# Kernel optimization log

Hardware: AMD Instinct MI355X
Metric: run time of the kernel (lower is better)

The kernel has to match this reference:

```python
import jax, jax.numpy as jnp
import numpy as np

ITER_STEPS = 2


def setup_inputs() -> dict:
    key = jax.random.key(0)
    ks = jax.random.split(key, 9)
    B, N, D, E = 64, 256, 512, 10  # batch, nodes, node_dim, edge types
    node = jax.random.normal(ks[0], (B, N, D), dtype=jnp.float32)
    node_mask = jax.random.randint(ks[1], (B, N), 0, 2).astype(jnp.int32)
    adj = jax.random.randint(ks[2], (E, B, N, N), 0, 2).astype(jnp.int32)
    s = 0.02
    W_nw = jax.random.normal(ks[3], (1, D), dtype=jnp.float32) * s   # node weight fc [out=1, in=D]
    b_nw = jnp.zeros((1,), dtype=jnp.float32)
    W_self = jax.random.normal(ks[4], (D, D), dtype=jnp.float32) * s
    b_self = jnp.zeros((D,), dtype=jnp.float32)
    W_edge = jax.random.normal(ks[5], (E, D, D), dtype=jnp.float32) * s  # per-edge-type Linear (no bias)
    return {"node": node, "W_nw": W_nw, "b_nw": b_nw, "W_self": W_self,
            "b_self": b_self, "W_edge": W_edge, "node_mask": node_mask, "adj": adj}


def reference(node, W_nw, b_nw, W_self, b_self, W_edge, node_mask, adj):
    # node: [B,N,D]; node_mask: [B,N] int; adj: [E=10,B,N,N] int (binary)
    B, N, D = node.shape
    m = node_mask.astype(node.dtype)
    eye = jnp.eye(N, dtype=node.dtype)
    # dd_graph = mask outer-product with zeroed diagonal: [B,N,N]
    dd = m[:, None, :] * m[:, :, None] * (1.0 - eye)
    graphs = dd[None] * adj.astype(node.dtype)  # [E,B,N,N]
    # total neighbor count across all 10 edge types, clamped to >=1 (replace_masked_values)
    neigh = graphs.sum(axis=(0, 3))                       # [B,N]
    neigh = jnp.where(neigh >= 1.0, neigh, 1.0)
    all_weight = []
    for _ in range(ITER_STEPS):
        # (1) node relatedness gate
        w = jax.nn.sigmoid(node @ W_nw.T + b_nw)[..., 0]  # [B,N]
        all_weight.append(w)
        self_info = node @ W_self.T + b_self              # [B,N,D]
        # (2) per-edge-type projection + masked adjacency matmul, summed over edge types
        proj = jnp.einsum('bnk,edk->ebnd', node, W_edge)  # [E,B,N,D]
        masked_w = jnp.where(graphs != 0, w[None, :, None, :], 0.0)  # [E,B,N,N]
        agg = jnp.einsum('ebnm,ebmd->bnd', masked_w, proj)           # [B,N,D]
        # (3) update
        node = jax.nn.relu(self_info + agg / neigh[..., None])
    return node, jnp.stack(all_weight, axis=1)  # ([B,N,D], [B,ITER,N])
```

## Files before the change

### kernel.cpp

```cpp
#include <hip/hip_runtime.h>
#include <hip/hip_bf16.h>

#define BB 64
#define NN 256
#define DD 512
#define EE 10

typedef __bf16 bf16x8 __attribute__((ext_vector_type(8)));
typedef unsigned short ushort8v __attribute__((ext_vector_type(8)));
typedef unsigned int uint4v __attribute__((ext_vector_type(4)));
typedef float floatx4 __attribute__((ext_vector_type(4)));
typedef float floatx16 __attribute__((ext_vector_type(16)));

typedef __attribute__((address_space(3))) unsigned short lds_us;
typedef const __attribute__((address_space(1))) unsigned short glb_us;

__device__ __forceinline__ unsigned short f2b(float f) {
    union { float f; unsigned u; } x; x.f = f;
    unsigned r = x.u + 0x7FFFu + ((x.u >> 16) & 1u);
    return (unsigned short)(r >> 16);
}
__device__ __forceinline__ float b2f(unsigned short u) {
    union { unsigned u; float f; } x; x.u = ((unsigned)u) << 16;
    return x.f;
}

__global__ void k_wconv(const float* __restrict__ W_edge,
                        const float* __restrict__ W_self,
                        unsigned short* __restrict__ Wf) {
    int t = blockIdx.x * 256 + threadIdx.x;
    int lane  = t & 63;
    int kstep = (t >> 6) & 31;
    int cfg   = (t >> 11) & 15;
    int e     = t >> 15;
    int dout = cfg * 32 + (lane & 31);
    int k    = kstep * 16 + (lane >> 5) * 8;
    const float* src = (e < EE) ? (W_edge + ((size_t)e * DD + dout) * DD + k)
                                : (W_self + (size_t)dout * DD + k);
    ushort8v o;
    #pragma unroll
    for (int j = 0; j < 8; j++) o[j] = f2b(src[j]);
    *(ushort8v*)(Wf + (size_t)t * 8) = o;
}

__global__ void k_graph(const int* __restrict__ adj, const int* __restrict__ mask,
                        unsigned* __restrict__ packed, float* __restrict__ recip) {
    int b = blockIdx.x >> 8;
    int n = blockIdx.x & 255;
    int lane = threadIdx.x & 63;
    int wv   = threadIdx.x >> 6;
    int m = wv * 64 + lane;
    int ok = (mask[b * NN + n] != 0) & (mask[b * NN + m] != 0) & (m != n);
    __shared__ int cnt_s[4];
    int total = 0;
    #pragma unroll
    for (int e = 0; e < EE; e++) {
        int a = adj[(((size_t)e * BB + b) * NN + n) * NN + m];
        int bit = ok & (a != 0);
        unsigned long long bal = __ballot(bit);
        if (lane == 0) {
            unsigned* dst = packed + (((size_t)e * BB + b) * NN + n) * 8 + wv * 2;
            dst[0] = (unsigned)bal;
            dst[1] = (unsigned)(bal >> 32);
        }
        total += bit;
    }
    for (int off = 32; off; off >>= 1) total += __shfl_down(total, off);
    if (lane == 0) cnt_s[wv] = total;
    __syncthreads();
    if (threadIdx.x == 0) {
        int c = cnt_s[0] + cnt_s[1] + cnt_s[2] + cnt_s[3];
        recip[b * NN + n] = 1.0f / (float)(c < 1 ? 1 : c);
    }
}

template<int TI>
__global__ void k_gate(const float* __restrict__ xf, const unsigned short* __restrict__ xbin,
                       const float* __restrict__ W_nw, const float* __restrict__ b_nw,
                       float* __restrict__ w_buf, float* __restrict__ w_out) {
    int idx = blockIdx.x * 4 + (threadIdx.x >> 6);
    int lane = threadIdx.x & 63;
    size_t base = (size_t)idx * DD + lane * 8;
    const floatx4* wp = (const floatx4*)(W_nw + lane * 8);
    floatx4 w0 = wp[0], w1 = wp[1];
    float s = 0.f;
    if (TI == 0) {
        const floatx4* xp = (const floatx4*)(xf + base);
        floatx4 a0 = xp[0], a1 = xp[1];
        #pragma unroll
        for (int j = 0; j < 4; j++) s += a0[j] * w0[j] + a1[j] * w1[j];
    } else {
        ushort8v u = *(const ushort8v*)(xbin + base);
        #pragma unroll
        for (int j = 0; j < 8; j++) {
            float wj = (j < 4) ? w0[j] : w1[j - 4];
            s += b2f(u[j]) * wj;
        }
    }
    for (int off = 32; off; off >>= 1) s += __shfl_down(s, off);
    if (lane == 0) {
        float v = 1.f / (1.f + __expf(-(s + b_nw[0])));
        w_buf[idx] = v;
        int b = idx >> 8, n = idx & 255;
        w_out[(b * 2 + TI) * NN + n] = v;
    }
}

template<int TI>
__global__ void k_transf(const float* __restrict__ xf, const unsigned short* __restrict__ xbin,
                         const float* __restrict__ w_buf,
                         unsigned short* __restrict__ wTf, unsigned short* __restrict__ xb0) {
    int bid = blockIdx.x;
    int b  = bid >> 5;
    int nt = (bid >> 3) & 3;
    int dt = bid & 7;
    __shared__ float tile[64][65];
    __shared__ float ws[64];
    int j  = threadIdx.x & 63;
    int i0 = threadIdx.x >> 6;
    if (threadIdx.x < 64) ws[threadIdx.x] = w_buf[b * NN + nt * 64 + threadIdx.x];
    #pragma unroll
    for (int ii = 0; ii < 16; ii++) {
        int i = i0 * 16 + ii;
        size_t gi = ((size_t)b * NN + nt * 64 + i) * DD + dt * 64 + j;
        float v = (TI == 0) ? xf[gi] : b2f(xbin[gi]);
        tile[i][j] = v;
        if (TI == 0) xb0[gi] = f2b(v);
    }
    __syncthreads();
    int lane = threadIdx.x & 63;
    int l31 = lane & 31, hi = lane >> 5;
    #pragma unroll
    for (int cc = 0; cc < 2; cc++) {
        int c = cc * 4 + (threadIdx.x >> 6);
        int msl = c >> 1, dbl = c & 1;
        ushort8v o;
        #pragma unroll
        for (int jj = 0; jj < 8; jj++) {
            int m_loc = msl * 16 + hi * 8 + jj;
            int d_loc = dbl * 32 + l31;
            o[jj] = f2b(tile[m_loc][d_loc] * ws[m_loc]);
        }
        size_t idx = (((size_t)b * 16 + nt * 4 + msl) * 16 + dt * 2 + dbl) * 64 + lane;
        *(ushort8v*)(wTf + idx * 8) = o;
    }
}

template<int TI>
__global__ __launch_bounds__(512, 2)
void k2_heavy(const unsigned short* __restrict__ wTf,
              const unsigned short* __restrict__ xb,
              const unsigned short* __restrict__ Wf,
              const unsigned* __restrict__ packed,
              const float* __restrict__ recip,
              const float* __restrict__ b_self,
              unsigned short* __restrict__ out_bf16,
              float* __restrict__ out_f32) {
    __shared__ __attribute__((aligned(16))) unsigned short sWT[32 * 512];
    __shared__ __attribute__((aligned(16))) unsigned short sWf[2][32 * 512];
    __shared__ __attribute__((aligned(16))) unsigned short sT[128 * 76];

    int bid = blockIdx.x;
    int xcd = bid & 7;
    int ct  = xcd >> 2;
    int rtile = (bid >> 3) * 4 + (xcd & 3);
    int b = rtile >> 1, h = rtile & 1;
    int w = threadIdx.x >> 6, lane = threadIdx.x & 63;
    int rh = w >> 2;
    int cq = w & 3;
    int rbT = rh * 2 + (cq >> 1);
    int cbT = cq & 1;
    int l31 = lane & 31, hi = lane >> 5;

    float rn[16];
    #pragma unroll
    for (int rg = 0; rg < 16; rg++) {
        int rloc = (rg & 3) + 8 * (rg >> 2) + 4 * hi;
        rn[rg] = recip[b * NN + h * 128 + rbT * 32 + rloc];
    }

    floatx16 acc2[2][2];
    #pragma unroll
    for (int i = 0; i < 2; i++)
        #pragma unroll
        for (int jj = 0; jj < 2; jj++)
            #pragma unroll
            for (int q = 0; q < 16; q++) acc2[i][jj][q] = 0.f;

    auto stage_sWf = [&](int e, int dc, int buf) {
        #pragma unroll
        for (int it = 0; it < 4; it++) {
            int c = it * 8 + w;
            int cfl = c >> 2, kl = c & 3;
            const unsigned short* g = Wf +
                ((((size_t)e * 16 + ct * 8 + cfl) * 32 + dc * 4 + kl) * 64 + lane) * 8;
            __builtin_amdgcn_global_load_lds((glb_us*)g, (lds_us*)&sWf[buf][c * 512], 16, 0, 0);
        }
    };
    auto stage_sWT = [&](int dc) {
        #pragma unroll
        for (int it = 0; it < 4; it++) {
            int c = it * 8 + w;
            int msl = c >> 1, dbl = c & 1;
            const unsigned short* g = wTf +
                ((((size_t)b * 16 + msl) * 16 + dc * 2 + dbl) * 64 + lane) * 8;
            __builtin_amdgcn_global_load_lds((glb_us*)g, (lds_us*)&sWT[c * 512], 16, 0, 0);
        }
    };

    stage_sWT(0);
    stage_sWf(0, 0, 0);

    bf16x8 Bc[16];

    #pragma unroll 1
    for (int dc = 0; dc < 8; dc++) {
        #pragma unroll 1
        for (int e = 0; e <= EE; e++) {
            int s = dc * 11 + e;
            int cur = s & 1;
            asm volatile("s_waitcnt vmcnt(0)" ::: "memory");
            asm volatile("s_barrier" ::: "memory");

            unsigned pw[8];
            ushort8v xa[2][4];
            if (e < EE) {
                const uint4v* pp = (const uint4v*)(packed +
                    (((size_t)e * BB + b) * NN + h * 128 + rbT * 32 + l31) * 8);
                uint4v pa = pp[0], pb = pp[1];
                pw[0]=pa[0]; pw[1]=pa[1]; pw[2]=pa[2]; pw[3]=pa[3];
                pw[4]=pb[0]; pw[5]=pb[1]; pw[6]=pb[2]; pw[7]=pb[3];
            } else {
                #pragma unroll
                for (int ra = 0; ra < 2; ra++)
                    #pragma unroll
                    for (int ks = 0; ks < 4; ks++)
                        xa[ra][ks] = *(const ushort8v*)(xb +
                            ((size_t)(b * NN + h * 128 + rh * 64 + ra * 32 + l31)) * DD +
                            dc * 64 + ks * 16 + hi * 8);
            }
            if (s < 87) {
                int ne = e + 1, ndc = dc;
                if (ne == 11) { ne = 0; ndc = dc + 1; }
                stage_sWf(ne, ndc, cur ^ 1);
            }
            if (e == 1 && dc < 7) stage_sWT(dc + 1);

            if (e == 0) {
                #pragma unroll
                for (int ms = 0; ms < 16; ms++)
                    Bc[ms] = __builtin_bit_cast(bf16x8,
                        *(const ushort8v*)&sWT[((ms * 2 + cbT) * 64 + lane) * 8]);
            }

            if (e < EE) {
                floatx16 acc3;
                #pragma unroll
                for (int q = 0; q < 16; q++) acc3[q] = 0.f;
                #pragma unroll
                for (int ms = 0; ms < 16; ms++) {
                    unsigned byte = (pw[ms >> 1] >> ((((ms & 1) << 1) + hi) * 8)) & 0xFFu;
                    uint4v av;
                    #pragma unroll
                    for (int p = 0; p < 4; p++) {
                        unsigned b2 = (byte >> (2 * p)) & 3u;
                        av[p] = ((b2 & 1u) ? 0x3F80u : 0u) | ((b2 & 2u) ? 0x3F800000u : 0u);
                    }
                    acc3 = __builtin_amdgcn_mfma_f32_32x32x16_bf16(
                        __builtin_bit_cast(bf16x8, av), Bc[ms], acc3, 0, 0, 0);
                }
                #pragma unroll
                for (int rg = 0; rg < 16; rg++) {
                    int rloc = rbT * 32 + (rg & 3) + 8 * (rg >> 2) + 4 * hi;
                    sT[rloc * 76 + cbT * 32 + l31] = f2b(acc3[rg] * rn[rg]);
                }
                asm volatile("s_waitcnt lgkmcnt(0)" ::: "memory");
                asm volatile("s_barrier" ::: "memory");
            }
            #pragma unroll
            for (int ks = 0; ks < 4; ks++) {
                bf16x8 bfr[2];
                #pragma unroll
                for (int cb = 0; cb < 2; cb++)
                    bfr[cb] = __builtin_bit_cast(bf16x8,
                        *(const ushort8v*)&sWf[cur][(((cq * 2 + cb) * 4 + ks) * 64 + lane) * 8]);
                #pragma unroll
                for (int ra = 0; ra < 2; ra++) {
                    bf16x8 afr;
                    if (e < EE)
                        afr = __builtin_bit_cast(bf16x8, *(const ushort8v*)
                            &sT[(rh * 64 + ra * 32 + l31) * 76 + ks * 16 + hi * 8]);
                    else
                        afr = __builtin_bit_cast(bf16x8, xa[ra][ks]);
                    #pragma unroll
                    for (int cb = 0; cb < 2; cb++)
                        acc2[ra][cb] = __builtin_amdgcn_mfma_f32_32x32x16_bf16(
                            afr, bfr[cb], acc2[ra][cb], 0, 0, 0);
                }
            }
        }
    }
    #pragma unroll
    for (int cb = 0; cb < 2; cb++) {
        int col = ct * 256 + (cq * 2 + cb) * 32 + l31;
        float bs = b_self[col];
        #pragma unroll
        for (int ra = 0; ra < 2; ra++) {
            #pragma unroll
            for (int rg = 0; rg < 16; rg++) {
                int row = h * 128 + rh * 64 + ra * 32 + (rg & 3) + 8 * (rg >> 2) + 4 * hi;
                float v = acc2[ra][cb][rg] + bs;
                v = v > 0.f ? v : 0.f;
                size_t gi = ((size_t)b * NN + row) * DD + col;
                if (TI == 0) out_bf16[gi] = f2b(v);
                else         out_f32[gi] = v;
            }
        }
    }
}

extern "C" void kernel_launch(void* const* d_in, const int* in_sizes, int n_in,
                              void* d_out, int out_size, void* d_ws, size_t ws_size,
                              hipStream_t stream) {
    const float* node   = (const float*)d_in[0];
    const float* W_nw   = (const float*)d_in[1];
    const float* b_nw   = (const float*)d_in[2];
    const float* W_self = (const float*)d_in[3];
    const float* b_self = (const float*)d_in[4];
    const float* W_edge = (const float*)d_in[5];
    const int*   mask   = (const int*)d_in[6];
    const int*   adj    = (const int*)d_in[7];
    float* out = (float*)d_out;
    float* out_w = out + (size_t)BB * NN * DD;

    char* ws = (char*)d_ws;
    size_t off = 0;
    unsigned short* Wf    = (unsigned short*)(ws + off); off += (size_t)11 * DD * DD * 2;
    unsigned short* wTf   = (unsigned short*)(ws + off); off += (size_t)BB * DD * NN * 2;
    unsigned short* xb0   = (unsigned short*)(ws + off); off += (size_t)BB * NN * DD * 2;
    unsigned short* xb1   = (unsigned short*)(ws + off); off += (size_t)BB * NN * DD * 2;
    unsigned*       packed= (unsigned*)(ws + off);       off += (size_t)EE * BB * NN * 8 * 4;
    float*          recip = (float*)(ws + off);          off += (size_t)BB * NN * 4;
    float*          w_buf = (float*)(ws + off);          off += (size_t)BB * NN * 4;

    k_wconv<<<dim3(1408), dim3(256), 0, stream>>>(W_edge, W_self, Wf);
    k_graph<<<dim3(16384), dim3(256), 0, stream>>>(adj, mask, packed, recip);

    k_gate<0><<<dim3(4096), dim3(256), 0, stream>>>(node, nullptr, W_nw, b_nw, w_buf, out_w);
    k_transf<0><<<dim3(2048), dim3(256), 0, stream>>>(node, nullptr, w_buf, wTf, xb0);
    k2_heavy<0><<<dim3(256), dim3(512), 0, stream>>>(wTf, xb0, Wf, packed, recip, b_self, xb1, nullptr);

    k_gate<1><<<dim3(4096), dim3(256), 0, stream>>>(nullptr, xb1, W_nw, b_nw, w_buf, out_w);
    k_transf<1><<<dim3(2048), dim3(256), 0, stream>>>(nullptr, xb1, w_buf, wTf, xb0 );
    k2_heavy<1><<<dim3(256), dim3(512), 0, stream>>>(wTf, xb1, Wf, packed, recip, b_self, nullptr, out);
}
```

Measured before the change: 794.8 us.

## Reorder heavy kernel loop edge-major, double-buffer wT tiles and swizzle sT LDS

The fused aggregate-then-project kernel now loops edge type outermost and d-chunk innermost. The adjacency bit-pattern fragments are decoded into registers once per edge type, and the wT tile is double-buffered and reloaded every step instead of being held in registers across edges. The first MFMA now transposes operand roles so each wave writes packed bf16 pairs to an XOR-swizzled 64-wide sT buffer rather than a padded one, which cuts LDS bank conflicts and scalar stores. Block-to-batch mapping changes from the XCD-aware layout to a simple b-major one, which may affect L2 locality. The self path reads xb directly from global memory inside the MFMA loop.

```diff
diff --git a/kernel.cpp b/kernel.cpp
--- a/kernel.cpp
+++ b/kernel.cpp
@@ -9,6 +9,7 @@
 typedef __bf16 bf16x8 __attribute__((ext_vector_type(8)));
 typedef unsigned short ushort8v __attribute__((ext_vector_type(8)));
 typedef unsigned int uint4v __attribute__((ext_vector_type(4)));
+typedef unsigned int uint2v __attribute__((ext_vector_type(2)));
 typedef float floatx4 __attribute__((ext_vector_type(4)));
 typedef float floatx16 __attribute__((ext_vector_type(16)));
 
@@ -23,6 +24,10 @@
 __device__ __forceinline__ float b2f(unsigned short u) {
     union { unsigned u; float f; } x; x.u = ((unsigned)u) << 16;
     return x.f;
+}
+__device__ __forceinline__ unsigned pack_bf16(float a, float b) {
+    union { float f; unsigned u; } xa, xb2; xa.f = a; xb2.f = b;
+    return __builtin_amdgcn_perm(xa.u + 0x8000u, xb2.u + 0x8000u, 0x07060302u);
 }
 
 __global__ void k_wconv(const float* __restrict__ W_edge,
@@ -156,28 +161,23 @@
               const float* __restrict__ b_self,
               unsigned short* __restrict__ out_bf16,
               float* __restrict__ out_f32) {
-    __shared__ __attribute__((aligned(16))) unsigned short sWT[32 * 512];
+    __shared__ __attribute__((aligned(16))) unsigned short sWT[2][32 * 512];
     __shared__ __attribute__((aligned(16))) unsigned short sWf[2][32 * 512];
-    __shared__ __attribute__((aligned(16))) unsigned short sT[128 * 76];
+    __shared__ __attribute__((aligned(16))) unsigned short sT[128 * 64];
 
     int bid = blockIdx.x;
-    int xcd = bid & 7;
-    int ct  = xcd >> 2;
-    int rtile = (bid >> 3) * 4 + (xcd & 3);
-    int b = rtile >> 1, h = rtile & 1;
+    int b  = bid & 63;
+    int q  = bid >> 6;
+    int h  = q >> 1;
+    int ct = q & 1;
     int w = threadIdx.x >> 6, lane = threadIdx.x & 63;
-    int rh = w >> 2;
-    int cq = w & 3;
-    int rbT = rh * 2 + (cq >> 1);
-    int cbT = cq & 1;
     int l31 = lane & 31, hi = lane >> 5;
-
-    float rn[16];
-    #pragma unroll
-    for (int rg = 0; rg < 16; rg++) {
-        int rloc = (rg & 3) + 8 * (rg >> 2) + 4 * hi;
-        rn[rg] = recip[b * NN + h * 128 + rbT * 32 + rloc];
-    }
+    int s1_d  = w & 1;
+    int s1_nb = w >> 1;
+    int n1 = s1_nb * 32 + l31;
+    float rn = recip[b * NN + h * 128 + n1];
+    int nh2 = w & 1;
+    int dh4 = w >> 1;
 
     floatx16 acc2[2][2];
     #pragma unroll
@@ -185,131 +185,132 @@
         #pragma unroll
         for (int jj = 0; jj < 2; jj++)
             #pragma unroll
-            for (int q = 0; q < 16; q++) acc2[i][jj][q] = 0.f;
-
-    auto stage_sWf = [&](int e, int dc, int buf) {
+            for (int p = 0; p < 16; p++) acc2[i][jj][p] = 0.f;
+
+    auto stage_sWT = [&](int dc, int buf) {
         #pragma unroll
         for (int it = 0; it < 4; it++) {
             int c = it * 8 + w;
-            int cfl = c >> 2, kl = c & 3;
-            const unsigned short* g = Wf +
-                ((((size_t)e * 16 + ct * 8 + cfl) * 32 + dc * 4 + kl) * 64 + lane) * 8;
-            __builtin_amdgcn_global_load_lds((glb_us*)g, (lds_us*)&sWf[buf][c * 512], 16, 0, 0);
+            const unsigned short* g = wTf +
+                ((((size_t)b * 16 + (c >> 1)) * 16 + dc * 2 + (c & 1)) * 64 + lane) * 8;
+            __builtin_amdgcn_global_load_lds((glb_us*)g, (lds_us*)&sWT[buf][c * 512], 16, 0, 0);
         }
     };
-    auto stage_sWT = [&](int dc) {
+    auto stage_sWf = [&](int e, int dc, int buf) {
         #pragma unroll
         for (int it = 0; it < 4; it++) {
             int c = it * 8 + w;
-            int msl = c >> 1, dbl = c & 1;
-            const unsigned short* g = wTf +
-                ((((size_t)b * 16 + msl) * 16 + dc * 2 + dbl) * 64 + lane) * 8;
-            __builtin_amdgcn_global_load_lds((glb_us*)g, (lds_us*)&sWT[c * 512], 16, 0, 0);
+            const unsigned short* g = Wf +
+                ((((size_t)e * 16 + ct * 8 + (c >> 2)) * 32 + dc * 4 + (c & 3)) * 64 + lane) * 8;
+            __builtin_amdgcn_global_load_lds((glb_us*)g, (lds_us*)&sWf[buf][c * 512], 16, 0, 0);
         }
     };
 
-    stage_sWT(0);
+    stage_sWT(0, 0);
     stage_sWf(0, 0, 0);
 
-    bf16x8 Bc[16];
+    bf16x8 Bg[16];
+    int swz1 = (n1 & 7) << 3;
 
     #pragma unroll 1
-    for (int dc = 0; dc < 8; dc++) {
-        #pragma unroll 1
-        for (int e = 0; e <= EE; e++) {
-            int s = dc * 11 + e;
-            int cur = s & 1;
-            asm volatile("s_waitcnt vmcnt(0)" ::: "memory");
-            asm volatile("s_barrier" ::: "memory");
-
-            unsigned pw[8];
-            ushort8v xa[2][4];
-            if (e < EE) {
+    for (int s = 0; s < 88; s++) {
+        int e = s >> 3, dc = s & 7, cur = s & 1;
+        asm volatile("s_waitcnt vmcnt(0)" ::: "memory");
+        asm volatile("s_barrier" ::: "memory");
+        if (s < 87) {
+            int ns = s + 1, ne = ns >> 3, ndc = ns & 7, nb = ns & 1;
+            if (ne < EE) stage_sWT(ndc, nb);
+            stage_sWf(ne, ndc, nb);
+        }
+        if (e < EE) {
+            if (dc == 0) {
                 const uint4v* pp = (const uint4v*)(packed +
-                    (((size_t)e * BB + b) * NN + h * 128 + rbT * 32 + l31) * 8);
+                    (((size_t)e * BB + b) * NN + h * 128 + n1) * 8);
                 uint4v pa = pp[0], pb = pp[1];
-                pw[0]=pa[0]; pw[1]=pa[1]; pw[2]=pa[2]; pw[3]=pa[3];
-                pw[4]=pb[0]; pw[5]=pb[1]; pw[6]=pb[2]; pw[7]=pb[3];
-            } else {
-                #pragma unroll
-                for (int ra = 0; ra < 2; ra++)
-                    #pragma unroll
-                    for (int ks = 0; ks < 4; ks++)
-                        xa[ra][ks] = *(const ushort8v*)(xb +
-                            ((size_t)(b * NN + h * 128 + rh * 64 + ra * 32 + l31)) * DD +
-                            dc * 64 + ks * 16 + hi * 8);
-            }
-            if (s < 87) {
-                int ne = e + 1, ndc = dc;
-                if (ne == 11) { ne = 0; ndc = dc + 1; }
-                stage_sWf(ne, ndc, cur ^ 1);
-            }
-            if (e == 1 && dc < 7) stage_sWT(dc + 1);
-
-            if (e == 0) {
-                #pragma unroll
-                for (int ms = 0; ms < 16; ms++)
-                    Bc[ms] = __builtin_bit_cast(bf16x8,
-                        *(const ushort8v*)&sWT[((ms * 2 + cbT) * 64 + lane) * 8]);
-            }
-
-            if (e < EE) {
-                floatx16 acc3;
-                #pragma unroll
-                for (int q = 0; q < 16; q++) acc3[q] = 0.f;
-                #pragma unroll
-                for (int ms = 0; ms < 16; ms++) {
-                    unsigned byte = (pw[ms >> 1] >> ((((ms & 1) << 1) + hi) * 8)) & 0xFFu;
+                unsigned pw[8] = {pa[0], pa[1], pa[2], pa[3], pb[0], pb[1], pb[2], pb[3]};
+                #pragma unroll
+                for (int ks = 0; ks < 16; ks++) {
+                    int byi = ks * 2 + hi;
+                    unsigned byte = (pw[byi >> 2] >> ((byi & 3) * 8)) & 0xFFu;
                     uint4v av;
                     #pragma unroll
                     for (int p = 0; p < 4; p++) {
-                        unsigned b2 = (byte >> (2 * p)) & 3u;
-                        av[p] = ((b2 & 1u) ? 0x3F80u : 0u) | ((b2 & 2u) ? 0x3F800000u : 0u);
+                        unsigned t = (byte >> (2 * p)) & 3u;
+                        unsigned u = (t | (t << 15)) & 0x10001u;
+                        av[p] = u * 0x3F80u;
                     }
-                    acc3 = __builtin_amdgcn_mfma_f32_32x32x16_bf16(
-                        __builtin_bit_cast(bf16x8, av), Bc[ms], acc3, 0, 0, 0);
+                    Bg[ks] = __builtin_bit_cast(bf16x8, av);
                 }
-                #pragma unroll
-                for (int rg = 0; rg < 16; rg++) {
-                    int rloc = rbT * 32 + (rg & 3) + 8 * (rg >> 2) + 4 * hi;
-                    sT[rloc * 76 + cbT * 32 + l31] = f2b(acc3[rg] * rn[rg]);
-                }
-                asm volatile("s_waitcnt lgkmcnt(0)" ::: "memory");
-                asm volatile("s_barrier" ::: "memory");
-            }
-            #pragma unroll
-            for (int ks = 0; ks < 4; ks++) {
+            }
+            floatx16 acc3;
+            #pragma unroll
+            for (int p = 0; p < 16; p++) acc3[p] = 0.f;
+            #pragma unroll
+            for (int ks = 0; ks < 16; ks++) {
+                bf16x8 afr = __builtin_bit_cast(bf16x8,
+                    *(const ushort8v*)&sWT[cur][(ks * 2 + s1_d) * 512 + lane * 8]);
+                acc3 = __builtin_amdgcn_mfma_f32_32x32x16_bf16(afr, Bg[ks], acc3, 0, 0, 0);
+            }
+            #pragma unroll
+            for (int qd = 0; qd < 4; qd++) {
+                int d0 = s1_d * 32 + qd * 8 + hi * 4;
+                uint2v pk;
+                pk[0] = pack_bf16(acc3[qd * 4 + 1] * rn, acc3[qd * 4 + 0] * rn);
+                pk[1] = pack_bf16(acc3[qd * 4 + 3] * rn, acc3[qd * 4 + 2] * rn);
+                *(uint2v*)&sT[n1 * 64 + (d0 ^ swz1)] = pk;
+            }
+            asm volatile("s_waitcnt lgkmcnt(0)" ::: "memory");
+            asm volatile("s_barrier" ::: "memory");
+            #pragma unroll
+            for (int kk = 0; kk < 4; kk++) {
                 bf16x8 bfr[2];
                 #pragma unroll
                 for (int cb = 0; cb < 2; cb++)
-                    bfr[cb] = __builtin_bit_cast(bf16x8,
-                        *(const ushort8v*)&sWf[cur][(((cq * 2 + cb) * 4 + ks) * 64 + lane) * 8]);
-                #pragma unroll
-                for (int ra = 0; ra < 2; ra++) {
-                    bf16x8 afr;
-                    if (e < EE)
-                        afr = __builtin_bit_cast(bf16x8, *(const ushort8v*)
-                            &sT[(rh * 64 + ra * 32 + l31) * 76 + ks * 16 + hi * 8]);
-                    else
-                        afr = __builtin_bit_cast(bf16x8, xa[ra][ks]);
+                    bfr[cb] = __builtin_bit_cast(bf16x8, *(const ushort8v*)
+                        &sWf[cur][((dh4 * 2 + cb) * 4 + kk) * 512 + lane * 8]);
+                #pragma unroll
+                for (int na = 0; na < 2; na++) {
+                    int nloc = nh2 * 64 + na * 32 + l31;
+                    int dloc = kk * 16 + hi * 8;
+                    bf16x8 afr = __builtin_bit_cast(bf16x8, *(const ushort8v*)
+                        &sT[nloc * 64 + (dloc ^ ((nloc & 7) << 3))]);
                     #pragma unroll
                     for (int cb = 0; cb < 2; cb++)
-                        acc2[ra][cb] = __builtin_amdgcn_mfma_f32_32x32x16_bf16(
-                            afr, bfr[cb], acc2[ra][cb], 0, 0, 0);
+                        acc2[na][cb] = __builtin_amdgcn_mfma_f32_32x32x16_bf16(
+                            afr, bfr[cb], acc2[na][cb], 0, 0, 0);
                 }
             }
+        } else {
+            #pragma unroll
+            for (int kk = 0; kk < 4; kk++) {
+                bf16x8 bfr[2];
+                #pragma unroll
+                for (int cb = 0; cb < 2; cb++)
+                    bfr[cb] = __builtin_bit_cast(bf16x8, *(const ushort8v*)
+                        &sWf[cur][((dh4 * 2 + cb) * 4 + kk) * 512 + lane * 8]);
+                #pragma unroll
+                for (int na = 0; na < 2; na++) {
+                    bf16x8 afr = __builtin_bit_cast(bf16x8, *(const ushort8v*)(xb +
+                        ((size_t)(b * NN + h * 128 + nh2 * 64 + na * 32 + l31)) * DD +
+                        dc * 64 + kk * 16 + hi * 8));
+                    #pragma unroll
+                    for (int cb = 0; cb < 2; cb++)
+                        acc2[na][cb] = __builtin_amdgcn_mfma_f32_32x32x16_bf16(
+                            afr, bfr[cb], acc2[na][cb], 0, 0, 0);
+                }
+            }
         }
     }
     #pragma unroll
     for (int cb = 0; cb < 2; cb++) {
-        int col = ct * 256 + (cq * 2 + cb) * 32 + l31;
+        int col = ct * 256 + dh4 * 64 + cb * 32 + l31;
         float bs = b_self[col];
         #pragma unroll
-        for (int ra = 0; ra < 2; ra++) {
+        for (int na = 0; na < 2; na++) {
             #pragma unroll
             for (int rg = 0; rg < 16; rg++) {
-                int row = h * 128 + rh * 64 + ra * 32 + (rg & 3) + 8 * (rg >> 2) + 4 * hi;
-                float v = acc2[ra][cb][rg] + bs;
+                int row = h * 128 + nh2 * 64 + na * 32 + (rg & 3) + 8 * (rg >> 2) + 4 * hi;
+                float v = acc2[na][cb][rg] + bs;
                 v = v > 0.f ? v : 0.f;
                 size_t gi = ((size_t)b * NN + row) * DD + col;
                 if (TI == 0) out_bf16[gi] = f2b(v);
```

Result: faster. 704.2 us (-11.4%).
